# Kernel tuning notes

Hardware: AMD Instinct MI355X
Metric: run time of the kernel (lower is better)

The kernel has to match this reference:

```python
import jax, jax.numpy as jnp
import numpy as np

B, S, D = 4, 2048, 2048
H, HD = 16, 128  # n_heads, head_dim; H*HD == D


def setup_inputs() -> dict:
    key = jax.random.key(0)
    ks = jax.random.split(key, 9)
    inp = {
        "q": jax.random.normal(ks[0], (B, S, D), dtype=jnp.float32),
        "k": jax.random.normal(ks[1], (B, S, D), dtype=jnp.float32),
        "v": jax.random.normal(ks[2], (B, S, D), dtype=jnp.float32),
        "attention_mask": jax.random.normal(ks[3], (S, S), dtype=jnp.float32),
        "key_padding_mask": jnp.zeros((B, S), dtype=jnp.float32),
        # torch nn.Linear weights are [out_features, in_features], bias=False
        "wq": jax.random.normal(ks[4], (H * HD, D), dtype=jnp.float32) * (1.0 / np.sqrt(D)),
        "wk": jax.random.normal(ks[5], (H * HD, D), dtype=jnp.float32) * (1.0 / np.sqrt(D)),
        "wv": jax.random.normal(ks[6], (H * HD, D), dtype=jnp.float32) * (1.0 / np.sqrt(D)),
        "wo": jax.random.normal(ks[7], (D, H * HD), dtype=jnp.float32) * (1.0 / np.sqrt(H * HD)),
    }
    return inp


def reference(q, k, v, attention_mask, key_padding_mask, wq, wk, wv, wo):
    # projections: x @ W.T, then split into heads -> [B, H, S, HD]
    def proj_heads(x, w):
        y = jnp.einsum('bsd,ed->bse', x, w)
        return y.reshape(B, S, H, HD).transpose(0, 2, 1, 3)

    qh = proj_heads(q, wq)
    kh = proj_heads(k, wk)
    vh = proj_heads(v, wv)

    scale = 1.0 / jnp.sqrt(jnp.asarray(HD, dtype=qh.dtype))
    scores = jnp.einsum('bhqd,bhkd->bhqk', qh, kh) * scale  # [B,H,S,S]
    scores = scores + attention_mask[None, None, :, :]       # additive 2D mask
    scores = scores + key_padding_mask[:, None, None, :]     # additive padding mask
    weights = jax.nn.softmax(scores, axis=-1)
    attn = jnp.einsum('bhqk,bhkd->bhqd', weights, vh)        # [B,H,S,HD]

    combined = attn.transpose(0, 2, 1, 3).reshape(B, S, H * HD)
    out = jnp.einsum('bse,de->bsd', combined, wo)
    return out
```

## Files before the change

kernel.cpp:

```cpp
#include <hip/hip_runtime.h>
#include <hip/hip_bf16.h>
#include <stdint.h>

#define S_LEN 2048
#define D_MODEL 2048
#define NH 16
#define HD_DIM 128
#define BATCH 4

typedef unsigned short u16;
typedef unsigned int u32;
typedef short s16x8 __attribute__((ext_vector_type(8)));
typedef float f32x4 __attribute__((ext_vector_type(4)));

__device__ __forceinline__ u16 f2b(float f) {
    union { float f; u32 u; } v; v.f = f;
    u32 r = v.u + 0x7FFFu + ((v.u >> 16) & 1u);
    return (u16)(r >> 16);
}

__device__ __forceinline__ u32 cvtpk(float lo, float hi) {
    u32 r;
    asm volatile("v_cvt_pk_bf16_f32 %0, %1, %2" : "=v"(r) : "v"(lo), "v"(hi));
    return r;
}

__device__ __forceinline__ float exp2a(float x) {
    float r;
    asm("v_exp_f32 %0, %1" : "=v"(r) : "v"(x));
    return r;
}
__device__ __forceinline__ float max3a(float a, float b, float c) {
    float r;
    asm("v_max3_f32 %0, %1, %2, %3" : "=v"(r) : "v"(a), "v"(b), "v"(c));
    return r;
}

#define L2E 1.4426950408889634f

#define BAR()   asm volatile("s_barrier" ::: "memory")
#define LGKM0() asm volatile("s_waitcnt lgkmcnt(0)" ::: "memory")
#define VMW(n)  asm volatile("s_waitcnt vmcnt(" #n ")" ::: "memory")

__global__ __launch_bounds__(256) void cvt_bf16(const float* __restrict__ in,
                                                u16* __restrict__ out, int n8) {
    int i = blockIdx.x * 256 + threadIdx.x;
    if (i >= n8) return;
    const float4* p = reinterpret_cast<const float4*>(in) + (size_t)i * 2;
    float4 a = p[0], b = p[1];
    s16x8 o;
    o[0] = (short)f2b(a.x); o[1] = (short)f2b(a.y);
    o[2] = (short)f2b(a.z); o[3] = (short)f2b(a.w);
    o[4] = (short)f2b(b.x); o[5] = (short)f2b(b.y);
    o[6] = (short)f2b(b.z); o[7] = (short)f2b(b.w);
    *(reinterpret_cast<s16x8*>(out) + i) = o;
}

__global__ __launch_bounds__(256) void cvt_w4(const float* __restrict__ s0,
                                              const float* __restrict__ s1,
                                              const float* __restrict__ s2,
                                              const float* __restrict__ s3,
                                              u16* __restrict__ out) {
    int i = blockIdx.x * 256 + threadIdx.x;
    const int seg = i >> 19, li = i & 524287;
    const float* s = (seg == 0) ? s0 : (seg == 1) ? s1 : (seg == 2) ? s2 : s3;
    const float4* p = reinterpret_cast<const float4*>(s) + (size_t)li * 2;
    float4 a = p[0], b = p[1];
    s16x8 o;
    o[0] = (short)f2b(a.x); o[1] = (short)f2b(a.y);
    o[2] = (short)f2b(a.z); o[3] = (short)f2b(a.w);
    o[4] = (short)f2b(b.x); o[5] = (short)f2b(b.y);
    o[6] = (short)f2b(b.z); o[7] = (short)f2b(b.w);
    *(reinterpret_cast<s16x8*>(out) + i) = o;
}

template<int OUT_MODE>
__global__ __launch_bounds__(512, 1) void gemm256(const u16* __restrict__ Ab,
                                                  const u16* __restrict__ Bw,
                                                  void* __restrict__ Cv,
                                                  int M, int N, int K, float alpha) {
    __shared__ u16 lds[2][2][256 * 64];
    const int t = threadIdx.x, lane = t & 63, w = t >> 6;
    const int wm = w >> 2, wn = w & 3;
    const int lr = lane & 15, lk = lane >> 4;
    const int NT = K >> 6;

    const int ntile = N >> 8;
    int flat = blockIdx.x;
    int cpx = gridDim.x >> 3;
    int rmap = (flat & 7) * cpx + (flat >> 3);
    const int m0 = (rmap / ntile) * 256, n0 = (rmap % ntile) * 256;

    const int srow = t >> 3;
    const int spos = t & 7;
    const int scon = spos ^ (srow & 7);

    auto stage = [&](const u16* gbase, int grow0, int ldsT, int buf, int q, int kt) {
        const u16* src = gbase + (size_t)(grow0 + q * 64 + srow) * K + kt * 64 + scon * 8;
        u16* dst = &lds[buf][ldsT][(q * 64 + srow) * 64 + spos * 8];
        __builtin_amdgcn_global_load_lds(
            (const __attribute__((address_space(1))) void*)src,
            (__attribute__((address_space(3))) void*)dst, 16, 0, 0);
    };

    f32x4 acc[8][4];
#pragma unroll
    for (int i = 0; i < 8; ++i)
#pragma unroll
        for (int j = 0; j < 4; ++j) acc[i][j] = {0.f, 0.f, 0.f, 0.f};

    s16x8 a[4][2], b[4][2];

    stage(Bw, n0, 1, 0, 0, 0);
    stage(Bw, n0, 1, 0, 1, 0);
    stage(Bw, n0, 1, 0, 2, 0);
    stage(Bw, n0, 1, 0, 3, 0);
    stage(Ab, m0, 0, 0, 0, 0);
    stage(Ab, m0, 0, 0, 2, 0);
    stage(Ab, m0, 0, 0, 1, 0);
    stage(Ab, m0, 0, 0, 3, 0);
    VMW(2);
    BAR();

#define LDFRAG(base, row, kk) \
    (*(const s16x8*)((base) + (row) * 64 + ((((kk) * 4 + lk) ^ (lr & 7)) << 3)))

#define QUAD(mh, nh)                                                                   \
    __builtin_amdgcn_s_setprio(1);                                                     \
    _Pragma("unroll")                                                                  \
    for (int mf = 0; mf < 4; ++mf)                                                     \
        _Pragma("unroll")                                                              \
        for (int nf = 0; nf < 2; ++nf)                                                 \
            _Pragma("unroll")                                                          \
            for (int kk = 0; kk < 2; ++kk)                                             \
                acc[(mh) * 4 + mf][(nh) * 2 + nf] = __builtin_amdgcn_mfma_f32_16x16x32_bf16( \
                    a[mf][kk], b[(nh) * 2 + nf][kk], acc[(mh) * 4 + mf][(nh) * 2 + nf], 0, 0, 0); \
    __builtin_amdgcn_s_setprio(0);

    for (int kt = 0; kt < NT; ++kt) {
        const int buf = kt & 1;
        const u16* la = &lds[buf][0][0];
        const u16* lb = &lds[buf][1][0];
        const int nx = kt + 1;
        const bool st = nx < NT;

#pragma unroll
        for (int mf = 0; mf < 4; ++mf)
#pragma unroll
            for (int kk = 0; kk < 2; ++kk)
                a[mf][kk] = LDFRAG(la, wm * 128 + mf * 16 + lr, kk);
#pragma unroll
        for (int nf = 0; nf < 2; ++nf)
#pragma unroll
            for (int kk = 0; kk < 2; ++kk)
                b[nf][kk] = LDFRAG(lb, wn * 64 + nf * 16 + lr, kk);
        if (st) { stage(Bw, n0, 1, buf ^ 1, 0, nx); stage(Bw, n0, 1, buf ^ 1, 1, nx); }
        BAR();
        LGKM0();
        QUAD(0, 0);
        BAR();

#pragma unroll
        for (int nf = 2; nf < 4; ++nf)
#pragma unroll
            for (int kk = 0; kk < 2; ++kk)
                b[nf][kk] = LDFRAG(lb, wn * 64 + nf * 16 + lr, kk);
        if (st) { stage(Bw, n0, 1, buf ^ 1, 2, nx); stage(Bw, n0, 1, buf ^ 1, 3, nx); }
        BAR();
        LGKM0();
        QUAD(0, 1);
        if (kt == NT - 1) { VMW(0); } else { VMW(4); }
        BAR();

#pragma unroll
        for (int mf = 0; mf < 4; ++mf)
#pragma unroll
            for (int kk = 0; kk < 2; ++kk)
                a[mf][kk] = LDFRAG(la, wm * 128 + 64 + mf * 16 + lr, kk);
        if (st) { stage(Ab, m0, 0, buf ^ 1, 0, nx); stage(Ab, m0, 0, buf ^ 1, 2, nx); }
        BAR();
        LGKM0();
        QUAD(1, 0);
        BAR();

        if (st) { stage(Ab, m0, 0, buf ^ 1, 1, nx); stage(Ab, m0, 0, buf ^ 1, 3, nx); }
        BAR();
        QUAD(1, 1);
        VMW(2);
        BAR();
    }

#pragma unroll
    for (int i = 0; i < 8; ++i)
#pragma unroll
        for (int j = 0; j < 4; ++j) {
            int r0 = m0 + wm * 128 + (i >> 2) * 64 + (i & 3) * 16 + lk * 4;
            int c0 = n0 + wn * 64 + j * 16 + lr;
            if constexpr (OUT_MODE == 1) {
                float* C = (float*)Cv;
#pragma unroll
                for (int r = 0; r < 4; ++r) C[(size_t)(r0 + r) * N + c0] = acc[i][j][r] * alpha;
            } else {
                u16* C = (u16*)Cv;
#pragma unroll
                for (int r = 0; r < 4; ++r) C[(size_t)(r0 + r) * N + c0] = f2b(acc[i][j][r] * alpha);
            }
        }
}

__global__ __launch_bounds__(512, 2) void attn_kernel(
    const u16* __restrict__ Qh, const u16* __restrict__ Kh, const u16* __restrict__ Vh,
    const float* __restrict__ mask, const float* __restrict__ kpad,
    u16* __restrict__ Comb) {
    __shared__ u16 Ks[2][64 * 128];
    __shared__ u16 Vt[2][128 * 64];

    const int t = threadIdx.x, lane = t & 63, w = t >> 6;
    const int lr = lane & 15, lk = lane >> 4;

    const int g = blockIdx.x;
    const int rm = (g & 7) * 64 + (g >> 3);
    const int qb = rm & 7, h = (rm >> 3) & 15, b = rm >> 7;
    const int q0w = qb * 256 + w * 32;
    const size_t rowBase = (size_t)b * S_LEN;
    const u16* Kb = Kh + rowBase * D_MODEL + h * HD_DIM;
    const u16* Vb = Vh + rowBase * D_MODEL + h * HD_DIM;

    s16x8 qf[2][4];
#pragma unroll
    for (int qi = 0; qi < 2; ++qi)
#pragma unroll
        for (int dc = 0; dc < 4; ++dc)
            qf[qi][dc] = *(const s16x8*)(Qh + (rowBase + q0w + qi * 16 + lr) * D_MODEL +
                                         h * HD_DIM + dc * 32 + lk * 8);

    f32x4 o[2][8];
#pragma unroll
    for (int qi = 0; qi < 2; ++qi)
#pragma unroll
        for (int dt = 0; dt < 8; ++dt) o[qi][dt] = {0.f, 0.f, 0.f, 0.f};
    float m_[2] = {-3e38f, -3e38f}, l_[2] = {0.f, 0.f};

    const int ksub = t >> 4;
    const int kchunk = (t & 15) ^ (ksub & 7);
    const int vrow = t >> 3;
    const int vc0 = (t & 7) * 16;
    const int vodd = vrow & 1;
    const int vp = t >> 4;

    s16x8 va0, va1;

    auto stageK = [&](int kv0, int nb) {
#pragma unroll
        for (int p = 0; p < 2; ++p) {
            const u16* src = Kb + (size_t)(kv0 + p * 32 + ksub) * D_MODEL + kchunk * 8;
            __builtin_amdgcn_global_load_lds(
                (const __attribute__((address_space(1))) void*)src,
                (__attribute__((address_space(3))) void*)(&Ks[nb][p * 4096 + t * 8]), 16, 0, 0);
        }
    };
    auto loadV = [&](int kv0) {
        const u16* p0 = Vb + (size_t)(kv0 + vrow) * D_MODEL + vc0;
        va0 = *(const s16x8*)p0;
        va1 = *(const s16x8*)(p0 + 8);
    };
    auto writeV = [&](int nb) {
        union VU { s16x8 v[2]; u32 uw[8]; u16 us[16]; };
        VU A;
        A.v[0] = va0; A.v[1] = va1;
        u32 ra[4];
#pragma unroll
        for (int i = 0; i < 4; ++i)
            ra[i] = (u32)__shfl_xor((int)(vodd ? A.uw[i] : A.uw[i + 4]), 8, 64);
#pragma unroll
        for (int e = 0; e < 8; ++e) {
            int d = vc0 + vodd * 8 + e;
            int swz = ((d >> 4) ^ (d & 7)) & 7;
            u16 rau = (u16)((ra[e >> 1] >> ((e & 1) * 16)) & 0xffff);
            u16 lo1, hi1;
            if (vodd) { lo1 = rau; hi1 = A.us[8 + e]; }
            else      { lo1 = A.us[e]; hi1 = rau; }
            int c1 = (vp >> 2) ^ swz;
            *(u32*)(&Vt[nb][d * 64 + c1 * 8 + (vp & 3) * 2]) = (u32)lo1 | ((u32)hi1 << 16);
        }
    };

    f32x4 mreg[2][4], kreg[4];
    auto loadMask = [&](int kv0) {
#pragma unroll
        for (int qi = 0; qi < 2; ++qi) {
            const float* mrow = mask + (size_t)(q0w + qi * 16 + lr) * S_LEN + kv0;
#pragma unroll
            for (int kt = 0; kt < 4; ++kt)
                mreg[qi][kt] = *(const f32x4*)(mrow + kt * 16 + lk * 4);
        }
#pragma unroll
        for (int kt = 0; kt < 4; ++kt)
            kreg[kt] = *(const f32x4*)(kpad + b * S_LEN + kv0 + kt * 16 + lk * 4);
    };

    stageK(0, 0);
    loadV(0);
    writeV(0);
    loadMask(0);
    __syncthreads();

    const int srcA = ((lk & 1) * 32) + lr;
    const int srcB = srcA + 16;

    for (int i = 0; i < 32; ++i) {
        const int cur = i & 1;
        const u16* ks = &Ks[cur][0];
        const u16* vt = &Vt[cur][0];
        const int kv0 = i * 64;

        if (i < 31) { stageK(kv0 + 64, cur ^ 1); loadV(kv0 + 64); }

        f32x4 sc[2][4];
#pragma unroll
        for (int qi = 0; qi < 2; ++qi)
#pragma unroll
            for (int kt = 0; kt < 4; ++kt) sc[qi][kt] = {0.f, 0.f, 0.f, 0.f};
        __builtin_amdgcn_s_setprio(1);
#pragma unroll
        for (int kt = 0; kt < 4; ++kt) {
            s16x8 kf[4];
#pragma unroll
            for (int dc = 0; dc < 4; ++dc)
                kf[dc] = *(const s16x8*)(&ks[(kt * 16 + lr) * 128 +
                                             (((dc * 4 + lk) ^ (lr & 7)) << 3)]);
#pragma unroll
            for (int dc = 0; dc < 4; ++dc) {
                sc[0][kt] = __builtin_amdgcn_mfma_f32_16x16x32_bf16(kf[dc], qf[0][dc], sc[0][kt], 0, 0, 0);
                sc[1][kt] = __builtin_amdgcn_mfma_f32_16x16x32_bf16(kf[dc], qf[1][dc], sc[1][kt], 0, 0, 0);
            }
        }
        __builtin_amdgcn_s_setprio(0);

        u32 lo[2][4], hi[2][4];
#pragma unroll
        for (int qi = 0; qi < 2; ++qi) {
            float s[16];
#pragma unroll
            for (int kt = 0; kt < 4; ++kt)
#pragma unroll
                for (int r = 0; r < 4; ++r)
                    s[kt * 4 + r] = fmaf(mreg[qi][kt][r], L2E,
                                         fmaf(kreg[kt][r], L2E, sc[qi][kt][r]));
            float t0 = max3a(s[0], s[1], s[2]);
            float t1 = max3a(s[3], s[4], s[5]);
            float t2 = max3a(s[6], s[7], s[8]);
            float t3 = max3a(s[9], s[10], s[11]);
            float t4 = max3a(s[12], s[13], s[14]);
            float mx = fmaxf(max3a(t0, t1, t2), max3a(t3, t4, s[15]));
            mx = fmaxf(mx, __shfl_xor(mx, 16, 64));
            mx = fmaxf(mx, __shfl_xor(mx, 32, 64));
            if (__any(mx > m_[qi] + 11.5f)) {
                float mn = fmaxf(m_[qi], mx);
                float fs = exp2a(m_[qi] - mn);
                m_[qi] = mn;
                l_[qi] *= fs;
#pragma unroll
                for (int r = 0; r < 4; ++r) {
                    float fsb = __shfl(fs, (lane & 48) | (lk * 4 + r), 64);
#pragma unroll
                    for (int dt = 0; dt < 8; ++dt) o[qi][dt][r] *= fsb;
                }
            }
            float ls = 0.f;
#pragma unroll
            for (int e = 0; e < 16; ++e) { s[e] = exp2a(s[e] - m_[qi]); ls += s[e]; }
            ls += __shfl_xor(ls, 16, 64);
            ls += __shfl_xor(ls, 32, 64);
            l_[qi] += ls;
#pragma unroll
            for (int kt = 0; kt < 4; ++kt) {
                lo[qi][kt] = cvtpk(s[kt * 4 + 0], s[kt * 4 + 1]);
                hi[qi][kt] = cvtpk(s[kt * 4 + 2], s[kt * 4 + 3]);
            }
        }

        if (i < 31) loadMask(kv0 + 64);

        s16x8 pf[2][2];
        const bool sel = (lk >> 1) & 1;
#pragma unroll
        for (int qi = 0; qi < 2; ++qi)
#pragma unroll
            for (int hh = 0; hh < 2; ++hh) {
                u32 w0a = (u32)__shfl((int)lo[qi][2 * hh], srcA, 64);
                u32 w0b = (u32)__shfl((int)lo[qi][2 * hh + 1], srcA, 64);
                u32 w1a = (u32)__shfl((int)hi[qi][2 * hh], srcA, 64);
                u32 w1b = (u32)__shfl((int)hi[qi][2 * hh + 1], srcA, 64);
                u32 w2a = (u32)__shfl((int)lo[qi][2 * hh], srcB, 64);
                u32 w2b = (u32)__shfl((int)lo[qi][2 * hh + 1], srcB, 64);
                u32 w3a = (u32)__shfl((int)hi[qi][2 * hh], srcB, 64);
                u32 w3b = (u32)__shfl((int)hi[qi][2 * hh + 1], srcB, 64);
                union { s16x8 v; u32 u[4]; } P;
                P.u[0] = sel ? w0b : w0a;
                P.u[1] = sel ? w1b : w1a;
                P.u[2] = sel ? w2b : w2a;
                P.u[3] = sel ? w3b : w3a;
                pf[qi][hh] = P.v;
            }

        __builtin_amdgcn_s_setprio(1);
#pragma unroll
        for (int dt = 0; dt < 8; ++dt) {
            int swz = dt ^ (lr & 7);
            s16x8 vf0 = *(const s16x8*)(&vt[(dt * 16 + lr) * 64 + ((lk ^ swz) << 3)]);
            s16x8 vf1 = *(const s16x8*)(&vt[(dt * 16 + lr) * 64 + (((4 + lk) ^ swz) << 3)]);
            o[0][dt] = __builtin_amdgcn_mfma_f32_16x16x32_bf16(pf[0][0], vf0, o[0][dt], 0, 0, 0);
            o[1][dt] = __builtin_amdgcn_mfma_f32_16x16x32_bf16(pf[1][0], vf0, o[1][dt], 0, 0, 0);
            o[0][dt] = __builtin_amdgcn_mfma_f32_16x16x32_bf16(pf[0][1], vf1, o[0][dt], 0, 0, 0);
            o[1][dt] = __builtin_amdgcn_mfma_f32_16x16x32_bf16(pf[1][1], vf1, o[1][dt], 0, 0, 0);
        }
        __builtin_amdgcn_s_setprio(0);

        if (i < 31) writeV(cur ^ 1);
        LGKM0();
        BAR();
    }

#pragma unroll
    for (int qi = 0; qi < 2; ++qi)
#pragma unroll
        for (int r = 0; r < 4; ++r) {
            float lb = __shfl(l_[qi], (lane & 48) | (lk * 4 + r), 64);
            float inv = 1.0f / lb;
            size_t row = rowBase + q0w + qi * 16 + lk * 4 + r;
            u16* dst = Comb + row * D_MODEL + h * HD_DIM + lr;
#pragma unroll
            for (int dt = 0; dt < 8; ++dt) dst[dt * 16] = f2b(o[qi][dt][r] * inv);
        }
}

extern "C" void kernel_launch(void* const* d_in, const int* in_sizes, int n_in,
                              void* d_out, int out_size, void* d_ws, size_t ws_size,
                              hipStream_t stream) {
    const float* q    = (const float*)d_in[0];
    const float* k    = (const float*)d_in[1];
    const float* v    = (const float*)d_in[2];
    const float* mask = (const float*)d_in[3];
    const float* kpad = (const float*)d_in[4];
    const float* wq   = (const float*)d_in[5];
    const float* wk   = (const float*)d_in[6];
    const float* wv   = (const float*)d_in[7];
    const float* wo   = (const float*)d_in[8];
    float* out = (float*)d_out;

    u16* wqb  = (u16*)d_ws;
    u16* wkb  = wqb + 4194304;
    u16* wvb  = wkb + 4194304;
    u16* wob  = wvb + 4194304;
    u16* qh   = wob + 4194304;
    u16* kh   = qh + 16777216;
    u16* vh   = kh + 16777216;
    u16* comb = vh + 16777216;

    const float scale = 0.08838834764831845f * 1.4426950408889634f;

    {
        int n8w = 4 * 524288;
        dim3 gw((n8w + 255) / 256);
        cvt_w4<<<gw, 256, 0, stream>>>(wq, wk, wv, wo, wqb);
    }
    int n8a = 16777216 / 8;
    dim3 ga((n8a + 255) / 256);
    dim3 gg((8192 / 256) * (2048 / 256));

    cvt_bf16<<<ga, 256, 0, stream>>>(q, comb, n8a);
    gemm256<0><<<gg, 512, 0, stream>>>(comb, wqb, qh, 8192, 2048, 2048, scale);
    cvt_bf16<<<ga, 256, 0, stream>>>(k, comb, n8a);
    gemm256<0><<<gg, 512, 0, stream>>>(comb, wkb, kh, 8192, 2048, 2048, 1.0f);
    cvt_bf16<<<ga, 256, 0, stream>>>(v, comb, n8a);
    gemm256<0><<<gg, 512, 0, stream>>>(comb, wvb, vh, 8192, 2048, 2048, 1.0f);

    attn_kernel<<<dim3(512), 512, 0, stream>>>(qh, kh, vh, mask, kpad, comb);

    gemm256<1><<<gg, 512, 0, stream>>>(comb, wob, out, 8192, 2048, 2048, 1.0f);
}
```

Measured before the change: 575.5 us.

## Fuse fp32-to-bf16 activation conversion into projection GEMM A-tile loading

```diff
diff --git a/kernel.cpp b/kernel.cpp
--- a/kernel.cpp
+++ b/kernel.cpp
@@ -21,7 +21,7 @@
 
 __device__ __forceinline__ u32 cvtpk(float lo, float hi) {
     u32 r;
-    asm volatile("v_cvt_pk_bf16_f32 %0, %1, %2" : "=v"(r) : "v"(lo), "v"(hi));
+    asm("v_cvt_pk_bf16_f32 %0, %1, %2" : "=v"(r) : "v"(lo), "v"(hi));
     return r;
 }
 
@@ -41,20 +41,6 @@
 #define BAR()   asm volatile("s_barrier" ::: "memory")
 #define LGKM0() asm volatile("s_waitcnt lgkmcnt(0)" ::: "memory")
 #define VMW(n)  asm volatile("s_waitcnt vmcnt(" #n ")" ::: "memory")
-
-__global__ __launch_bounds__(256) void cvt_bf16(const float* __restrict__ in,
-                                                u16* __restrict__ out, int n8) {
-    int i = blockIdx.x * 256 + threadIdx.x;
-    if (i >= n8) return;
-    const float4* p = reinterpret_cast<const float4*>(in) + (size_t)i * 2;
-    float4 a = p[0], b = p[1];
-    s16x8 o;
-    o[0] = (short)f2b(a.x); o[1] = (short)f2b(a.y);
-    o[2] = (short)f2b(a.z); o[3] = (short)f2b(a.w);
-    o[4] = (short)f2b(b.x); o[5] = (short)f2b(b.y);
-    o[6] = (short)f2b(b.z); o[7] = (short)f2b(b.w);
-    *(reinterpret_cast<s16x8*>(out) + i) = o;
-}
 
 __global__ __launch_bounds__(256) void cvt_w4(const float* __restrict__ s0,
                                               const float* __restrict__ s1,
@@ -74,8 +60,8 @@
     *(reinterpret_cast<s16x8*>(out) + i) = o;
 }
 
-template<int OUT_MODE>
-__global__ __launch_bounds__(512, 1) void gemm256(const u16* __restrict__ Ab,
+template<int A_F32, int OUT_F32>
+__global__ __launch_bounds__(512, 1) void gemm256(const void* __restrict__ Av,
                                                   const u16* __restrict__ Bw,
                                                   void* __restrict__ Cv,
                                                   int M, int N, int K, float alpha) {
@@ -85,6 +71,9 @@
     const int lr = lane & 15, lk = lane >> 4;
     const int NT = K >> 6;
 
+    const u16* Ab = (const u16*)Av;
+    const float* Af = (const float*)Av;
+
     const int ntile = N >> 8;
     int flat = blockIdx.x;
     int cpx = gridDim.x >> 3;
@@ -103,6 +92,21 @@
             (__attribute__((address_space(3))) void*)dst, 16, 0, 0);
     };
 
+    f32x4 areg[4][2];
+    auto loadA = [&](int q, int kt) {
+        const float* src = Af + (size_t)(m0 + q * 64 + srow) * K + kt * 64 + scon * 8;
+        areg[q][0] = *(const f32x4*)(src);
+        areg[q][1] = *(const f32x4*)(src + 4);
+    };
+    auto writeA = [&](int buf, int q) {
+        union { s16x8 v; u32 u[4]; } o;
+        o.u[0] = cvtpk(areg[q][0][0], areg[q][0][1]);
+        o.u[1] = cvtpk(areg[q][0][2], areg[q][0][3]);
+        o.u[2] = cvtpk(areg[q][1][0], areg[q][1][1]);
+        o.u[3] = cvtpk(areg[q][1][2], areg[q][1][3]);
+        *(s16x8*)(&lds[buf][0][(q * 64 + srow) * 64 + spos * 8]) = o.v;
+    };
+
     f32x4 acc[8][4];
 #pragma unroll
     for (int i = 0; i < 8; ++i)
@@ -111,16 +115,28 @@
 
     s16x8 a[4][2], b[4][2];
 
-    stage(Bw, n0, 1, 0, 0, 0);
-    stage(Bw, n0, 1, 0, 1, 0);
-    stage(Bw, n0, 1, 0, 2, 0);
-    stage(Bw, n0, 1, 0, 3, 0);
-    stage(Ab, m0, 0, 0, 0, 0);
-    stage(Ab, m0, 0, 0, 2, 0);
-    stage(Ab, m0, 0, 0, 1, 0);
-    stage(Ab, m0, 0, 0, 3, 0);
-    VMW(2);
-    BAR();
+    if constexpr (A_F32) {
+        stage(Bw, n0, 1, 0, 0, 0);
+        stage(Bw, n0, 1, 0, 1, 0);
+        stage(Bw, n0, 1, 0, 2, 0);
+        stage(Bw, n0, 1, 0, 3, 0);
+        loadA(0, 0); loadA(1, 0); loadA(2, 0); loadA(3, 0);
+        writeA(0, 0); writeA(0, 1); writeA(0, 2); writeA(0, 3);
+        VMW(0);
+        LGKM0();
+        BAR();
+    } else {
+        stage(Bw, n0, 1, 0, 0, 0);
+        stage(Bw, n0, 1, 0, 1, 0);
+        stage(Bw, n0, 1, 0, 2, 0);
+        stage(Bw, n0, 1, 0, 3, 0);
+        stage(Ab, m0, 0, 0, 0, 0);
+        stage(Ab, m0, 0, 0, 2, 0);
+        stage(Ab, m0, 0, 0, 1, 0);
+        stage(Ab, m0, 0, 0, 3, 0);
+        VMW(2);
+        BAR();
+    }
 
 #define LDFRAG(base, row, kk) \
     (*(const s16x8*)((base) + (row) * 64 + ((((kk) * 4 + lk) ^ (lr & 7)) << 3)))
@@ -154,7 +170,11 @@
 #pragma unroll
             for (int kk = 0; kk < 2; ++kk)
                 b[nf][kk] = LDFRAG(lb, wn * 64 + nf * 16 + lr, kk);
-        if (st) { stage(Bw, n0, 1, buf ^ 1, 0, nx); stage(Bw, n0, 1, buf ^ 1, 1, nx); }
+        if (st) {
+            if constexpr (A_F32) { loadA(0, nx); loadA(1, nx); }
+            stage(Bw, n0, 1, buf ^ 1, 0, nx);
+            stage(Bw, n0, 1, buf ^ 1, 1, nx);
+        }
         BAR();
         LGKM0();
         QUAD(0, 0);
@@ -165,11 +185,17 @@
 #pragma unroll
             for (int kk = 0; kk < 2; ++kk)
                 b[nf][kk] = LDFRAG(lb, wn * 64 + nf * 16 + lr, kk);
-        if (st) { stage(Bw, n0, 1, buf ^ 1, 2, nx); stage(Bw, n0, 1, buf ^ 1, 3, nx); }
+        if (st) {
+            if constexpr (A_F32) { loadA(2, nx); loadA(3, nx); }
+            stage(Bw, n0, 1, buf ^ 1, 2, nx);
+            stage(Bw, n0, 1, buf ^ 1, 3, nx);
+        }
         BAR();
         LGKM0();
         QUAD(0, 1);
-        if (kt == NT - 1) { VMW(0); } else { VMW(4); }
+        if constexpr (!A_F32) {
+            if (kt == NT - 1) { VMW(0); } else { VMW(4); }
+        }
         BAR();
 
 #pragma unroll
@@ -177,16 +203,27 @@
 #pragma unroll
             for (int kk = 0; kk < 2; ++kk)
                 a[mf][kk] = LDFRAG(la, wm * 128 + 64 + mf * 16 + lr, kk);
-        if (st) { stage(Ab, m0, 0, buf ^ 1, 0, nx); stage(Ab, m0, 0, buf ^ 1, 2, nx); }
+        if (st) {
+            if constexpr (A_F32) { writeA(buf ^ 1, 0); writeA(buf ^ 1, 1); }
+            else { stage(Ab, m0, 0, buf ^ 1, 0, nx); stage(Ab, m0, 0, buf ^ 1, 2, nx); }
+        }
         BAR();
         LGKM0();
         QUAD(1, 0);
         BAR();
 
-        if (st) { stage(Ab, m0, 0, buf ^ 1, 1, nx); stage(Ab, m0, 0, buf ^ 1, 3, nx); }
+        if (st) {
+            if constexpr (A_F32) { writeA(buf ^ 1, 2); writeA(buf ^ 1, 3); }
+            else { stage(Ab, m0, 0, buf ^ 1, 1, nx); stage(Ab, m0, 0, buf ^ 1, 3, nx); }
+        }
         BAR();
         QUAD(1, 1);
-        VMW(2);
+        if constexpr (A_F32) {
+            LGKM0();
+            VMW(0);
+        } else {
+            VMW(2);
+        }
         BAR();
     }
 
@@ -196,7 +233,7 @@
         for (int j = 0; j < 4; ++j) {
             int r0 = m0 + wm * 128 + (i >> 2) * 64 + (i & 3) * 16 + lk * 4;
             int c0 = n0 + wn * 64 + j * 16 + lr;
-            if constexpr (OUT_MODE == 1) {
+            if constexpr (OUT_F32) {
                 float* C = (float*)Cv;
 #pragma unroll
                 for (int r = 0; r < 4; ++r) C[(size_t)(r0 + r) * N + c0] = acc[i][j][r] * alpha;
@@ -465,18 +502,13 @@
         dim3 gw((n8w + 255) / 256);
         cvt_w4<<<gw, 256, 0, stream>>>(wq, wk, wv, wo, wqb);
     }
-    int n8a = 16777216 / 8;
-    dim3 ga((n8a + 255) / 256);
     dim3 gg((8192 / 256) * (2048 / 256));
 
-    cvt_bf16<<<ga, 256, 0, stream>>>(q, comb, n8a);
-    gemm256<0><<<gg, 512, 0, stream>>>(comb, wqb, qh, 8192, 2048, 2048, scale);
-    cvt_bf16<<<ga, 256, 0, stream>>>(k, comb, n8a);
-    gemm256<0><<<gg, 512, 0, stream>>>(comb, wkb, kh, 8192, 2048, 2048, 1.0f);
-    cvt_bf16<<<ga, 256, 0, stream>>>(v, comb, n8a);
-    gemm256<0><<<gg, 512, 0, stream>>>(comb, wvb, vh, 8192, 2048, 2048, 1.0f);
+    gemm256<1, 0><<<gg, 512, 0, stream>>>(q, wqb, qh, 8192, 2048, 2048, scale);
+    gemm256<1, 0><<<gg, 512, 0, stream>>>(k, wkb, kh, 8192, 2048, 2048, 1.0f);
+    gemm256<1, 0><<<gg, 512, 0, stream>>>(v, wvb, vh, 8192, 2048, 2048, 1.0f);
 
     attn_kernel<<<dim3(512), 512, 0, stream>>>(qh, kh, vh, mask, kpad, comb);
 
-    gemm256<1><<<gg, 512, 0, stream>>>(comb, wob, out, 8192, 2048, 2048, 1.0f);
-}
+    gemm256<0, 1><<<gg, 512, 0, stream>>>(comb, wob, out, 8192, 2048, 2048, 1.0f);
+}
```

Result: slower. 723.6 us (+25.7%).
